# Performance work log

Hardware: AMD Instinct MI355X
Metric: run time of the kernel (lower is better)

Reference implementation:

```python
import jax, jax.numpy as jnp
import numpy as np

B, T, D, M = 4, 4096, 1024, 1024
EPS = 1e-6


def _rms_norm(x, w):
    return x * jax.lax.rsqrt(jnp.mean(x * x, axis=-1, keepdims=True) + EPS) * w


def _linrec(xg, r, h0):
    # h_t = x_t + r_t * h_{t-1}  (SRU-style linear recurrence, sqrll_kernel)
    def step(h, inp):
        xt, rt = inp
        h = xt + rt * h
        return h, h
    _, ys = jax.lax.scan(step, h0, (jnp.swapaxes(xg, 0, 1), jnp.swapaxes(r, 0, 1)))
    return jnp.swapaxes(ys, 0, 1)  # [B,T,M]


def setup_inputs() -> dict:
    key = jax.random.key(0)
    ks = jax.random.split(key, 16)
    s = 0.02
    return {
        "x": jax.random.normal(ks[0], (B, T, D), jnp.float32),
        "mem": jnp.zeros((B, M), jnp.float32),
        "norm_w": jnp.ones((D,), jnp.float32),
        "wr_w": jax.random.normal(ks[1], (M, D), jnp.float32) * s,
        "wr_b": jnp.zeros((M,), jnp.float32),
        "wi_w": jax.random.normal(ks[2], (M, D), jnp.float32) * s,
        "wig_w": jax.random.normal(ks[3], (M, D), jnp.float32) * s,
        "wig_b": jnp.zeros((M,), jnp.float32),
        "wog_w": jax.random.normal(ks[4], (M, D), jnp.float32) * s,
        "wog_b": jnp.zeros((M,), jnp.float32),
        "wo_w": jax.random.normal(ks[5], (D, M), jnp.float32) * s,
        "ffnorm_w": jnp.ones((D,), jnp.float32),
        "ffn_wi_w": jax.random.normal(ks[6], (M, D), jnp.float32) * s,
        "ffn_wg_w": jax.random.normal(ks[7], (M, D), jnp.float32) * s,
        "ffn_wg_b": jnp.zeros((M,), jnp.float32),
        "ffn_wo_w": jax.random.normal(ks[8], (D, M), jnp.float32) * s,
    }


def reference(x, mem, norm_w, wr_w, wr_b, wi_w, wig_w, wig_b, wog_w, wog_b,
              wo_w, ffnorm_w, ffn_wi_w, ffn_wg_w, ffn_wg_b, ffn_wo_w):
    # --- sqrll branch ---
    y = _rms_norm(x, norm_w)                                   # [B,T,D]
    ig = jax.nn.sigmoid(jnp.einsum('btd,md->btm', y, wig_w) + wig_b)
    og = jax.nn.sigmoid(jnp.einsum('btd,md->btm', y, wog_w) + wog_b)
    r = jax.nn.sigmoid(jnp.einsum('btd,md->btm', y, wr_w) + wr_b)
    xg = jnp.einsum('btd,md->btm', y, wi_w) * ig               # gated input
    h = _linrec(xg, r, mem)                                    # [B,T,M]
    mem_out = jax.lax.stop_gradient(h[:, -1])
    s = (h / (1.0 + jnp.abs(h))) * og                          # softsign * out gate
    x = x + jnp.einsum('btm,dm->btd', s, wo_w)                 # residual (dropout=0)
    # --- gated FFN branch ---
    z = _rms_norm(x, ffnorm_w)
    ff = jnp.einsum('btd,md->btm', z, ffn_wi_w) * jax.nn.sigmoid(
        jnp.einsum('btd,md->btm', z, ffn_wg_w) + ffn_wg_b)
    x = x + jnp.einsum('btm,dm->btd', ff, ffn_wo_w)
    return (x, mem_out)
```

## Files before the change

### kernel.cpp

```cpp
#include <hip/hip_runtime.h>
#include <stdint.h>


#define R_ROWS 16384
#define DIM    1024
#define MDIM   1024
#define TSEQ   4096
#define NCHUNK 128
#define TCH    32

typedef __attribute__((ext_vector_type(8))) short  bf16x8;
typedef __attribute__((ext_vector_type(8))) ushort u16x8;
typedef __attribute__((ext_vector_type(4))) float  f32x4;

__device__ __forceinline__ float bf2f(ushort u) {
  union { float f; unsigned int i; } x; x.i = ((unsigned int)u) << 16; return x.f;
}
__device__ __forceinline__ ushort f2bf(float f) {
  union { float f; unsigned int i; } x; x.f = f;
  unsigned int r = x.i + 0x7fffu + ((x.i >> 16) & 1u);
  return (ushort)(r >> 16);
}
__device__ __forceinline__ float sigmoidf_(float x) {
  return 1.0f / (1.0f + __expf(-x));
}
__device__ __forceinline__ void load_lds16(const void* g, void* s) {
  __builtin_amdgcn_global_load_lds(
      (const __attribute__((address_space(1))) void*)g,
      (__attribute__((address_space(3))) void*)s, 16, 0, 0);
}

#define AOFF(s,h) ((((s)*2)+(h))*8192)
#define BOFF(s,h) (49152 + (((s)*2)+(h))*8192)

__global__ __launch_bounds__(256)
void cvt_weights(const float* __restrict__ w0, const float* __restrict__ w1,
                 const float* __restrict__ w2, const float* __restrict__ w3,
                 const float* __restrict__ w4, const float* __restrict__ w5,
                 const float* __restrict__ w6, ushort* __restrict__ dst)
{
  const float* src; size_t base; int il;
  switch (blockIdx.y) {
    case 0: src = w0; base = 0;       il = 0; break;
    case 1: src = w1; base = 1048576; il = 0; break;
    case 2: src = w2; base = 2097152; il = 1; break;
    case 3: src = w3; base = 2097152; il = 2; break;
    case 4: src = w4; base = 5242880; il = 1; break;
    case 5: src = w5; base = 5242880; il = 2; break;
    default: src = w6; base = 4194304; il = 0; break;
  }
  const int i = blockIdx.x * 256 + threadIdx.x;
  const size_t e = (size_t)i * 4;
  size_t off;
  if (il == 0) off = base + e;
  else {
    const int row = (int)(e >> 10), col = (int)(e & 1023);
    const int nr = ((row >> 7) << 8) + (row & 127) + (il == 2 ? 128 : 0);
    off = base + (size_t)nr * 1024 + col;
  }
  const float4 v = *(const float4*)(src + e);
  ushort4 o; o.x = f2bf(v.x); o.y = f2bf(v.y); o.z = f2bf(v.z); o.w = f2bf(v.w);
  *(ushort4*)(dst + off) = o;
}

__global__ __launch_bounds__(256)
void cvt_one(const float* __restrict__ src, ushort* __restrict__ dst)
{
  const int i = blockIdx.x * 256 + threadIdx.x;
  const float4 v = *(const float4*)(src + (size_t)i * 4);
  ushort4 o; o.x = f2bf(v.x); o.y = f2bf(v.y); o.z = f2bf(v.z); o.w = f2bf(v.w);
  *(ushort4*)(dst + (size_t)i * 4) = o;
}

template<bool IN_F32>
__global__ __launch_bounds__(256)
void rmsnorm_k(const void* __restrict__ xin, const float* __restrict__ w,
               ushort* __restrict__ y)
{
  __shared__ float red[4];
  const int row = blockIdx.x;
  const int tid = threadIdx.x;
  const size_t base = (size_t)row * DIM + tid * 4;
  float v[4];
  if (IN_F32) {
    const float4 xv = *(const float4*)((const float*)xin + base);
    v[0] = xv.x; v[1] = xv.y; v[2] = xv.z; v[3] = xv.w;
  } else {
    const ushort4 xv = *(const ushort4*)((const ushort*)xin + base);
    v[0] = bf2f(xv.x); v[1] = bf2f(xv.y); v[2] = bf2f(xv.z); v[3] = bf2f(xv.w);
  }
  float ss = v[0]*v[0] + v[1]*v[1] + v[2]*v[2] + v[3]*v[3];
  for (int o = 32; o > 0; o >>= 1) ss += __shfl_down(ss, o, 64);
  const int wave = tid >> 6, lane = tid & 63;
  if (lane == 0) red[wave] = ss;
  __syncthreads();
  const float sum = red[0] + red[1] + red[2] + red[3];
  const float scale = rsqrtf(sum * (1.0f / DIM) + 1e-6f);
  const float4 wv = *(const float4*)(w + tid * 4);
  ushort4 o4;
  o4.x = f2bf(v[0] * scale * wv.x);
  o4.y = f2bf(v[1] * scale * wv.y);
  o4.z = f2bf(v[2] * scale * wv.z);
  o4.w = f2bf(v[3] * scale * wv.w);
  *(ushort4*)(y + base) = o4;
}

template<int MODE>
__global__ __launch_bounds__(512, 2)
void gemm8(const ushort* __restrict__ A, const ushort* __restrict__ W,
           const float* __restrict__ bias, const float* __restrict__ auxf,
           const ushort* __restrict__ auxb, ushort* __restrict__ outb,
           float* __restrict__ outf,
           const float* __restrict__ bias2, const float* __restrict__ bias3,
           ushort* __restrict__ outb2, ushort* __restrict__ outb3)
{
  __shared__ __align__(16) ushort lds[81920];
  const int tid  = threadIdx.x;
  const int bm = blockIdx.x, bn = blockIdx.y;
  const int wave = tid >> 6, lane = tid & 63;
  const int wm = wave >> 2, wn = wave & 3;
  const int quad = lane >> 4, l16 = lane & 15;
  const int axor = l16 & 7;

  const ushort* Ab = A + (size_t)bm * (256 * 1024);
  const ushort* Wb = W + (size_t)bn * (256 * 1024);

  f32x4 acc[8][4];
#pragma unroll
  for (int i = 0; i < 8; ++i)
#pragma unroll
    for (int j = 0; j < 4; ++j) acc[i][j] = (f32x4){0.f, 0.f, 0.f, 0.f};

  const int ci0 = tid, ci1 = tid + 512;
  const size_t gs0 = (size_t)(ci0 >> 3) * 1024 + (size_t)(((ci0 & 7) ^ ((ci0 >> 3) & 7)) << 3);
  const size_t gs1 = (size_t)(ci1 >> 3) * 1024 + (size_t)(((ci1 & 7) ^ ((ci1 >> 3) & 7)) << 3);
  auto stage = [&](const ushort* __restrict__ src, int loff) {
    load_lds16(src + gs0, &lds[loff + ci0 * 8]);
    load_lds16(src + gs1, &lds[loff + ci1 * 8]);
  };

  stage(Ab,               AOFF(0,0));
  stage(Ab + 131072,      AOFF(0,1));
  stage(Wb,               BOFF(0,0));
  stage(Wb + 131072,      BOFF(0,1));
  stage(Ab + 64,          AOFF(1,0));
  stage(Ab + 131072 + 64, AOFF(1,1));
  stage(Wb + 64,          BOFF(1,0));
  asm volatile("s_waitcnt vmcnt(6)" ::: "memory");
  __builtin_amdgcn_s_barrier();

  int kt3 = 0;
  for (int kt = 0; kt < 16; ++kt) {
    const ushort* Ah = &lds[AOFF(kt3, wm)];
    const ushort* Bh = &lds[BOFF(kt & 1, wn >> 1)];
    const int kt2s = (kt3 >= 1) ? kt3 - 1 : 2;
    const int brow0 = (wn & 1) * 64;
    bf16x8 bfr[4][2];
#pragma unroll
    for (int q = 0; q < 4; ++q) {
      if (q == 0) {
#pragma unroll
        for (int j = 0; j < 4; ++j)
#pragma unroll
          for (int ks = 0; ks < 2; ++ks)
            bfr[j][ks] = *(const bf16x8*)
                &Bh[(brow0 + j * 16 + l16) * 64 +
                    (((ks * 4 + quad) ^ axor) << 3)];
      }
      bf16x8 af[2][2];
#pragma unroll
      for (int p = 0; p < 2; ++p)
#pragma unroll
        for (int ks = 0; ks < 2; ++ks)
          af[p][ks] = *(const bf16x8*)
              &Ah[((2 * q + p) * 16 + l16) * 64 +
                  (((ks * 4 + quad) ^ axor) << 3)];
      if (q == 0 && kt + 1 < 16)
        stage(Wb + 131072 + (kt + 1) * 64, BOFF((kt + 1) & 1, 1));
      if (q == 1 && kt + 2 < 16)
        stage(Ab + (kt + 2) * 64,          AOFF(kt2s, 0));
      if (q == 2 && kt + 2 < 16)
        stage(Ab + 131072 + (kt + 2) * 64, AOFF(kt2s, 1));
      if (q == 3) {
        if (kt + 2 < 16)
          stage(Wb + (kt + 2) * 64,        BOFF(kt & 1, 0));
        if (kt < 14)       asm volatile("s_waitcnt vmcnt(6)" ::: "memory");
        else if (kt == 14) asm volatile("s_waitcnt vmcnt(0)" ::: "memory");
      }
      __builtin_amdgcn_s_barrier();
      asm volatile("s_waitcnt lgkmcnt(0)" ::: "memory");
      __builtin_amdgcn_s_setprio(1);
#pragma unroll
      for (int p = 0; p < 2; ++p)
#pragma unroll
        for (int j = 0; j < 4; ++j)
#pragma unroll
          for (int ks = 0; ks < 2; ++ks)
            acc[2 * q + p][j] = __builtin_amdgcn_mfma_f32_16x16x32_bf16(
                af[p][ks], bfr[j][ks], acc[2 * q + p][j], 0, 0, 0);
      __builtin_amdgcn_s_setprio(0);
    }
    kt3 = (kt3 == 2) ? 0 : kt3 + 1;
  }

  __builtin_amdgcn_s_barrier();
  float* C = (float*)lds;
  const bool gated = (MODE == 5) || (MODE == 6 && bn >= 8);
#pragma unroll 1
  for (int h = 0; h < 2; ++h) {
    if (wm == h) {
      const int cb = wn * 64;
#pragma unroll
      for (int i = 0; i < 8; ++i)
#pragma unroll
        for (int j = 0; j < 4; ++j)
#pragma unroll
          for (int g = 0; g < 4; ++g) {
            const int rw = i * 16 + quad * 4 + g;
            const int cw = cb + j * 16 + l16;
            C[rw * 256 + (cw ^ (((rw >> 2) & 1) << 4))] = acc[i][j][g];
          }
    }
    __syncthreads();
    if (gated) {
      const int outcol = (MODE == 6) ? (bn - 8) * 128 : bn * 128;
      const float* bp = (MODE == 6) ? bias3 : bias;
      ushort* ob = (MODE == 6) ? outb3 : outb;
#pragma unroll 1
      for (int sp = 0; sp < 4; ++sp) {
        const int lin = sp * 4096 + tid * 8;
        const int row = lin >> 7, c8 = lin & 127;
        const int xr = ((row >> 2) & 1) << 4;
        const int cg = c8 ^ xr;
        const int cv = (c8 + 128) ^ xr;
        const float4 gA = *(const float4*)&C[row * 256 + cg];
        const float4 gB = *(const float4*)&C[row * 256 + cg + 4];
        const float4 vA = *(const float4*)&C[row * 256 + cv];
        const float4 vB = *(const float4*)&C[row * 256 + cv + 4];
        const float4 b0 = *(const float4*)(bp + outcol + c8);
        const float4 b1 = *(const float4*)(bp + outcol + c8 + 4);
        const int rg = bm * 256 + h * 128 + row;
        const size_t gidx = (size_t)rg * 1024 + outcol + c8;
        u16x8 o;
        o[0] = f2bf(vA.x * sigmoidf_(gA.x + b0.x));
        o[1] = f2bf(vA.y * sigmoidf_(gA.y + b0.y));
        o[2] = f2bf(vA.z * sigmoidf_(gA.z + b0.z));
        o[3] = f2bf(vA.w * sigmoidf_(gA.w + b0.w));
        o[4] = f2bf(vB.x * sigmoidf_(gB.x + b1.x));
        o[5] = f2bf(vB.y * sigmoidf_(gB.y + b1.y));
        o[6] = f2bf(vB.z * sigmoidf_(gB.z + b1.z));
        o[7] = f2bf(vB.w * sigmoidf_(gB.w + b1.w));
        *(u16x8*)(ob + gidx) = o;
      }
    } else {
#pragma unroll 1
      for (int sp = 0; sp < 8; ++sp) {
        const int lin = sp * 4096 + tid * 8;
        const int row = lin >> 8, c8 = lin & 255;
        const int xr = ((row >> 2) & 1) << 4;
        const int cx = c8 ^ xr;
        const float4 vA = *(const float4*)&C[row * 256 + cx];
        const float4 vB = *(const float4*)&C[row * 256 + cx + 4];
        const int rg = bm * 256 + h * 128 + row;
        if (MODE == 6) {
          const int grp = bn >> 2;
          ushort* ob = grp ? outb2 : outb;
          const float* bp = grp ? bias2 : bias;
          const int colbase = (bn & 3) * 256;
          const size_t gidx = (size_t)rg * 1024 + colbase + c8;
          const float4 b0 = *(const float4*)(bp + colbase + c8);
          const float4 b1 = *(const float4*)(bp + colbase + c8 + 4);
          u16x8 o;
          o[0] = f2bf(sigmoidf_(vA.x + b0.x)); o[1] = f2bf(sigmoidf_(vA.y + b0.y));
          o[2] = f2bf(sigmoidf_(vA.z + b0.z)); o[3] = f2bf(sigmoidf_(vA.w + b0.w));
          o[4] = f2bf(sigmoidf_(vB.x + b1.x)); o[5] = f2bf(sigmoidf_(vB.y + b1.y));
          o[6] = f2bf(sigmoidf_(vB.z + b1.z)); o[7] = f2bf(sigmoidf_(vB.w + b1.w));
          *(u16x8*)(ob + gidx) = o;
        } else if (MODE == 1) {
          const size_t gidx = (size_t)rg * 1024 + bn * 256 + c8;
          const float4 a0 = *(const float4*)(auxf + gidx);
          const float4 a1 = *(const float4*)(auxf + gidx + 4);
          u16x8 o;
          o[0] = f2bf(vA.x + a0.x); o[1] = f2bf(vA.y + a0.y);
          o[2] = f2bf(vA.z + a0.z); o[3] = f2bf(vA.w + a0.w);
          o[4] = f2bf(vB.x + a1.x); o[5] = f2bf(vB.y + a1.y);
          o[6] = f2bf(vB.z + a1.z); o[7] = f2bf(vB.w + a1.w);
          *(u16x8*)(outb + gidx) = o;
        } else {
          const size_t gidx = (size_t)rg * 1024 + bn * 256 + c8;
          const u16x8 a8 = *(const u16x8*)(auxb + gidx);
          float4 o0, o1;
          o0.x = vA.x + bf2f(a8[0]); o0.y = vA.y + bf2f(a8[1]);
          o0.z = vA.z + bf2f(a8[2]); o0.w = vA.w + bf2f(a8[3]);
          o1.x = vB.x + bf2f(a8[4]); o1.y = vB.y + bf2f(a8[5]);
          o1.z = vB.z + bf2f(a8[6]); o1.w = vB.w + bf2f(a8[7]);
          *(float4*)(outf + gidx) = o0;
          *(float4*)(outf + gidx + 4) = o1;
        }
      }
    }
    if (h == 0) __syncthreads();
  }
}

__global__ __launch_bounds__(256)
void linrec_passA(ushort* __restrict__ xg, const ushort* __restrict__ r,
                  float* __restrict__ cL, float* __restrict__ cP)
{
  const int g = blockIdx.x * 256 + threadIdx.x;
  const int m4 = (g & 255) << 2;
  const int bc = g >> 8;
  const int b = bc >> 7, c = bc & 127;
  const size_t base = ((size_t)(b * TSEQ + c * TCH)) * MDIM + m4;
  float h0 = 0.f, h1 = 0.f, h2 = 0.f, h3 = 0.f;
  float p0 = 1.f, p1 = 1.f, p2 = 1.f, p3 = 1.f;
  for (int t = 0; t < TCH; ++t) {
    const size_t idx = base + (size_t)t * MDIM;
    const ushort4 xv = *(const ushort4*)&xg[idx];
    const ushort4 rv = *(const ushort4*)&r[idx];
    const float r0 = bf2f(rv.x), r1 = bf2f(rv.y), r2 = bf2f(rv.z), r3 = bf2f(rv.w);
    h0 = fmaf(r0, h0, bf2f(xv.x)); p0 *= r0;
    h1 = fmaf(r1, h1, bf2f(xv.y)); p1 *= r1;
    h2 = fmaf(r2, h2, bf2f(xv.z)); p2 *= r2;
    h3 = fmaf(r3, h3, bf2f(xv.w)); p3 *= r3;
    ushort4 o; o.x = f2bf(h0); o.y = f2bf(h1); o.z = f2bf(h2); o.w = f2bf(h3);
    *(ushort4*)&xg[idx] = o;
  }
  const size_t cb = (size_t)c * 4096 + b * MDIM + m4;
  float4 L4; L4.x = h0; L4.y = h1; L4.z = h2; L4.w = h3;
  float4 P4; P4.x = p0; P4.y = p1; P4.z = p2; P4.w = p3;
  *(float4*)&cL[cb] = L4;
  *(float4*)&cP[cb] = P4;
}

__global__ __launch_bounds__(256)
void linrec_passB(const float* __restrict__ cL, const float* __restrict__ cP,
                  const float* __restrict__ mem, float* __restrict__ cIn,
                  float* __restrict__ memout)
{
  const int g = blockIdx.x * 256 + threadIdx.x;
  float carry = mem[g];
#pragma unroll 4
  for (int c = 0; c < NCHUNK; ++c) {
    cIn[c * 4096 + g] = carry;
    carry = fmaf(cP[c * 4096 + g], carry, cL[c * 4096 + g]);
  }
  memout[g] = carry;
}

__global__ __launch_bounds__(256)
void linrec_passC(const ushort* __restrict__ L, const ushort* __restrict__ r,
                  const ushort* __restrict__ og, const float* __restrict__ cIn,
                  ushort* __restrict__ s)
{
  const int g = blockIdx.x * 256 + threadIdx.x;
  const int m4 = (g & 255) << 2;
  const int bc = g >> 8;
  const int b = bc >> 7, c = bc & 127;
  const size_t base = ((size_t)(b * TSEQ + c * TCH)) * MDIM + m4;
  const size_t cb = (size_t)c * 4096 + b * MDIM + m4;
  const float4 ci = *(const float4*)&cIn[cb];
  float p0 = 1.f, p1 = 1.f, p2 = 1.f, p3 = 1.f;
  for (int t = 0; t < TCH; ++t) {
    const size_t idx = base + (size_t)t * MDIM;
    const ushort4 rv = *(const ushort4*)&r[idx];
    const ushort4 lv = *(const ushort4*)&L[idx];
    const ushort4 ov = *(const ushort4*)&og[idx];
    p0 *= bf2f(rv.x); p1 *= bf2f(rv.y); p2 *= bf2f(rv.z); p3 *= bf2f(rv.w);
    const float a0 = fmaf(p0, ci.x, bf2f(lv.x));
    const float a1 = fmaf(p1, ci.y, bf2f(lv.y));
    const float a2 = fmaf(p2, ci.z, bf2f(lv.z));
    const float a3 = fmaf(p3, ci.w, bf2f(lv.w));
    ushort4 o;
    o.x = f2bf(a0 / (1.0f + fabsf(a0)) * bf2f(ov.x));
    o.y = f2bf(a1 / (1.0f + fabsf(a1)) * bf2f(ov.y));
    o.z = f2bf(a2 / (1.0f + fabsf(a2)) * bf2f(ov.z));
    o.w = f2bf(a3 / (1.0f + fabsf(a3)) * bf2f(ov.w));
    *(ushort4*)&s[idx] = o;
  }
}

extern "C" void kernel_launch(void* const* d_in, const int* in_sizes, int n_in,
                              void* d_out, int out_size, void* d_ws, size_t ws_size,
                              hipStream_t stream)
{
  const float* x        = (const float*)d_in[0];
  const float* mem      = (const float*)d_in[1];
  const float* norm_w   = (const float*)d_in[2];
  const float* wr_w     = (const float*)d_in[3];
  const float* wr_b     = (const float*)d_in[4];
  const float* wi_w     = (const float*)d_in[5];
  const float* wig_w    = (const float*)d_in[6];
  const float* wig_b    = (const float*)d_in[7];
  const float* wog_w    = (const float*)d_in[8];
  const float* wog_b    = (const float*)d_in[9];
  const float* wo_w     = (const float*)d_in[10];
  const float* ffnorm_w = (const float*)d_in[11];
  const float* ffn_wi_w = (const float*)d_in[12];
  const float* ffn_wg_w = (const float*)d_in[13];
  const float* ffn_wg_b = (const float*)d_in[14];
  const float* ffn_wo_w = (const float*)d_in[15];
  float* outF = (float*)d_out;

  ushort* xgL  = (ushort*)d_out;
  ushort* wbf  = (ushort*)((char*)d_out + 33554432ULL);
  float*  cL   = (float*)((char*)d_out + 48234496ULL);
  float*  cP   = (float*)((char*)d_out + 50331648ULL);
  float*  cIn  = (float*)((char*)d_out + 52428800ULL);
  float*  memoutF = outF + 16777216;

  char* ws = (char*)d_ws;
  ushort* y   = (ushort*)(ws);
  ushort* r   = (ushort*)(ws + 33554432ULL);
  ushort* og  = (ushort*)(ws + 67108864ULL);
  ushort* fwo_bf = (ushort*)(ws + 100663296ULL);
  ushort* s   = y;
  ushort* x1  = og;
  ushort* z   = r;
  ushort* gf  = y;

  cvt_weights<<<dim3(1024, 7), 256, 0, stream>>>(
      wr_w, wog_w, wig_w, wi_w, ffn_wg_w, ffn_wi_w, wo_w, wbf);
  cvt_one<<<1024, 256, 0, stream>>>(ffn_wo_w, fwo_bf);

  rmsnorm_k<true><<<R_ROWS, 256, 0, stream>>>(x, norm_w, y);
  gemm8<6><<<dim3(64, 16), 512, 0, stream>>>(
      y, wbf, wr_b, nullptr, nullptr, r, nullptr, wog_b, wig_b, og, xgL);
  linrec_passA<<<512, 256, 0, stream>>>(xgL, r, cL, cP);
  linrec_passB<<<16, 256, 0, stream>>>(cL, cP, mem, cIn, memoutF);
  linrec_passC<<<512, 256, 0, stream>>>(xgL, r, og, cIn, s);
  gemm8<1><<<dim3(64, 4), 512, 0, stream>>>(
      s, wbf + 4194304, nullptr, x, nullptr, x1, nullptr,
      nullptr, nullptr, nullptr, nullptr);
  rmsnorm_k<false><<<R_ROWS, 256, 0, stream>>>(x1, ffnorm_w, z);
  gemm8<5><<<dim3(64, 8), 512, 0, stream>>>(
      z, wbf + 5242880, ffn_wg_b, nullptr, nullptr, gf, nullptr,
      nullptr, nullptr, nullptr, nullptr);
  gemm8<3><<<dim3(64, 4), 512, 0, stream>>>(
      gf, fwo_bf, nullptr, nullptr, x1, nullptr, outF,
      nullptr, nullptr, nullptr, nullptr);
}
```

Measured before the change: 530.1 us.

## Switch GEMM to 32x32x16 MFMA, widen rmsnorm rows, merge weight conversion

The GEMM inner loop moves from 16x16x32 to 32x32x16 bf16 MFMA tiles. Fragment loads and the accumulator layout change to match, and the XOR swizzle in the epilogue LDS staging is dropped. The aim is fewer MFMA issues and LDS reads per FLOP, at the risk of LDS bank conflicts on the unswizzled C writes. Separately, rmsnorm processes two rows per block with 8-wide vectors, the two weight-conversion kernels are merged into one launch, and passB is relaunched with smaller blocks spread over more CUs.

```diff
diff --git a/kernel.cpp b/kernel.cpp
--- a/kernel.cpp
+++ b/kernel.cpp
@@ -9,9 +9,10 @@
 #define NCHUNK 128
 #define TCH    32
 
-typedef __attribute__((ext_vector_type(8))) short  bf16x8;
-typedef __attribute__((ext_vector_type(8))) ushort u16x8;
-typedef __attribute__((ext_vector_type(4))) float  f32x4;
+typedef __attribute__((ext_vector_type(8)))  short  bf16x8;
+typedef __attribute__((ext_vector_type(8)))  ushort u16x8;
+typedef __attribute__((ext_vector_type(4)))  float  f32x4;
+typedef __attribute__((ext_vector_type(16))) float  f32x16;
 
 __device__ __forceinline__ float bf2f(ushort u) {
   union { float f; unsigned int i; } x; x.i = ((unsigned int)u) << 16; return x.f;
@@ -37,9 +38,10 @@
 void cvt_weights(const float* __restrict__ w0, const float* __restrict__ w1,
                  const float* __restrict__ w2, const float* __restrict__ w3,
                  const float* __restrict__ w4, const float* __restrict__ w5,
-                 const float* __restrict__ w6, ushort* __restrict__ dst)
-{
-  const float* src; size_t base; int il;
+                 const float* __restrict__ w6, const float* __restrict__ w7,
+                 ushort* __restrict__ dst, ushort* __restrict__ dst2)
+{
+  const float* src; size_t base; int il; ushort* d = dst;
   switch (blockIdx.y) {
     case 0: src = w0; base = 0;       il = 0; break;
     case 1: src = w1; base = 1048576; il = 0; break;
@@ -47,7 +49,8 @@
     case 3: src = w3; base = 2097152; il = 2; break;
     case 4: src = w4; base = 5242880; il = 1; break;
     case 5: src = w5; base = 5242880; il = 2; break;
-    default: src = w6; base = 4194304; il = 0; break;
+    case 6: src = w6; base = 4194304; il = 0; break;
+    default: src = w7; base = 0; il = 0; d = dst2; break;
   }
   const int i = blockIdx.x * 256 + threadIdx.x;
   const size_t e = (size_t)i * 4;
@@ -60,16 +63,7 @@
   }
   const float4 v = *(const float4*)(src + e);
   ushort4 o; o.x = f2bf(v.x); o.y = f2bf(v.y); o.z = f2bf(v.z); o.w = f2bf(v.w);
-  *(ushort4*)(dst + off) = o;
-}
-
-__global__ __launch_bounds__(256)
-void cvt_one(const float* __restrict__ src, ushort* __restrict__ dst)
-{
-  const int i = blockIdx.x * 256 + threadIdx.x;
-  const float4 v = *(const float4*)(src + (size_t)i * 4);
-  ushort4 o; o.x = f2bf(v.x); o.y = f2bf(v.y); o.z = f2bf(v.z); o.w = f2bf(v.w);
-  *(ushort4*)(dst + (size_t)i * 4) = o;
+  *(ushort4*)(d + off) = o;
 }
 
 template<bool IN_F32>
@@ -78,31 +72,39 @@
                ushort* __restrict__ y)
 {
   __shared__ float red[4];
-  const int row = blockIdx.x;
   const int tid = threadIdx.x;
-  const size_t base = (size_t)row * DIM + tid * 4;
-  float v[4];
+  const int rh = tid >> 7;
+  const int rr = tid & 127;
+  const int row = blockIdx.x * 2 + rh;
+  const size_t base = (size_t)row * DIM + rr * 8;
+  float v[8];
   if (IN_F32) {
-    const float4 xv = *(const float4*)((const float*)xin + base);
-    v[0] = xv.x; v[1] = xv.y; v[2] = xv.z; v[3] = xv.w;
+    const float4 a = *(const float4*)((const float*)xin + base);
+    const float4 b = *(const float4*)((const float*)xin + base + 4);
+    v[0]=a.x; v[1]=a.y; v[2]=a.z; v[3]=a.w;
+    v[4]=b.x; v[5]=b.y; v[6]=b.z; v[7]=b.w;
   } else {
-    const ushort4 xv = *(const ushort4*)((const ushort*)xin + base);
-    v[0] = bf2f(xv.x); v[1] = bf2f(xv.y); v[2] = bf2f(xv.z); v[3] = bf2f(xv.w);
-  }
-  float ss = v[0]*v[0] + v[1]*v[1] + v[2]*v[2] + v[3]*v[3];
+    const u16x8 xv = *(const u16x8*)((const ushort*)xin + base);
+#pragma unroll
+    for (int i = 0; i < 8; ++i) v[i] = bf2f(xv[i]);
+  }
+  float ss = 0.f;
+#pragma unroll
+  for (int i = 0; i < 8; ++i) ss += v[i] * v[i];
   for (int o = 32; o > 0; o >>= 1) ss += __shfl_down(ss, o, 64);
-  const int wave = tid >> 6, lane = tid & 63;
-  if (lane == 0) red[wave] = ss;
+  const int wave = tid >> 6;
+  if ((tid & 63) == 0) red[wave] = ss;
   __syncthreads();
-  const float sum = red[0] + red[1] + red[2] + red[3];
+  const float sum = red[rh * 2] + red[rh * 2 + 1];
   const float scale = rsqrtf(sum * (1.0f / DIM) + 1e-6f);
-  const float4 wv = *(const float4*)(w + tid * 4);
-  ushort4 o4;
-  o4.x = f2bf(v[0] * scale * wv.x);
-  o4.y = f2bf(v[1] * scale * wv.y);
-  o4.z = f2bf(v[2] * scale * wv.z);
-  o4.w = f2bf(v[3] * scale * wv.w);
-  *(ushort4*)(y + base) = o4;
+  const float4 wa = *(const float4*)(w + rr * 8);
+  const float4 wb = *(const float4*)(w + rr * 8 + 4);
+  u16x8 o;
+  o[0] = f2bf(v[0] * scale * wa.x); o[1] = f2bf(v[1] * scale * wa.y);
+  o[2] = f2bf(v[2] * scale * wa.z); o[3] = f2bf(v[3] * scale * wa.w);
+  o[4] = f2bf(v[4] * scale * wb.x); o[5] = f2bf(v[5] * scale * wb.y);
+  o[6] = f2bf(v[6] * scale * wb.z); o[7] = f2bf(v[7] * scale * wb.w);
+  *(u16x8*)(y + base) = o;
 }
 
 template<int MODE>
@@ -119,17 +121,18 @@
   const int bm = blockIdx.x, bn = blockIdx.y;
   const int wave = tid >> 6, lane = tid & 63;
   const int wm = wave >> 2, wn = wave & 3;
-  const int quad = lane >> 4, l16 = lane & 15;
-  const int axor = l16 & 7;
+  const int l31 = lane & 31, lhi = lane >> 5, l7 = lane & 7;
 
   const ushort* Ab = A + (size_t)bm * (256 * 1024);
   const ushort* Wb = W + (size_t)bn * (256 * 1024);
 
-  f32x4 acc[8][4];
-#pragma unroll
-  for (int i = 0; i < 8; ++i)
-#pragma unroll
-    for (int j = 0; j < 4; ++j) acc[i][j] = (f32x4){0.f, 0.f, 0.f, 0.f};
+  f32x16 acc[4][2];
+#pragma unroll
+  for (int i = 0; i < 4; ++i)
+#pragma unroll
+    for (int j = 0; j < 2; ++j)
+#pragma unroll
+      for (int k = 0; k < 16; ++k) acc[i][j][k] = 0.f;
 
   const int ci0 = tid, ci1 = tid + 512;
   const size_t gs0 = (size_t)(ci0 >> 3) * 1024 + (size_t)(((ci0 & 7) ^ ((ci0 >> 3) & 7)) << 3);
@@ -155,26 +158,23 @@
     const ushort* Bh = &lds[BOFF(kt & 1, wn >> 1)];
     const int kt2s = (kt3 >= 1) ? kt3 - 1 : 2;
     const int brow0 = (wn & 1) * 64;
-    bf16x8 bfr[4][2];
+    bf16x8 bfa[4][2];
 #pragma unroll
     for (int q = 0; q < 4; ++q) {
       if (q == 0) {
 #pragma unroll
-        for (int j = 0; j < 4; ++j)
-#pragma unroll
-          for (int ks = 0; ks < 2; ++ks)
-            bfr[j][ks] = *(const bf16x8*)
-                &Bh[(brow0 + j * 16 + l16) * 64 +
-                    (((ks * 4 + quad) ^ axor) << 3)];
+        for (int qq = 0; qq < 4; ++qq)
+#pragma unroll
+          for (int nt = 0; nt < 2; ++nt)
+            bfa[qq][nt] = *(const bf16x8*)
+                &Bh[(brow0 + nt * 32 + l31) * 64 +
+                    (((qq * 2 + lhi) ^ l7) << 3)];
       }
-      bf16x8 af[2][2];
-#pragma unroll
-      for (int p = 0; p < 2; ++p)
-#pragma unroll
-        for (int ks = 0; ks < 2; ++ks)
-          af[p][ks] = *(const bf16x8*)
-              &Ah[((2 * q + p) * 16 + l16) * 64 +
-                  (((ks * 4 + quad) ^ axor) << 3)];
+      bf16x8 af[4];
+#pragma unroll
+      for (int mt = 0; mt < 4; ++mt)
+        af[mt] = *(const bf16x8*)
+            &Ah[(mt * 32 + l31) * 64 + (((q * 2 + lhi) ^ l7) << 3)];
       if (q == 0 && kt + 1 < 16)
         stage(Wb + 131072 + (kt + 1) * 64, BOFF((kt + 1) & 1, 1));
       if (q == 1 && kt + 2 < 16)
@@ -191,13 +191,11 @@
       asm volatile("s_waitcnt lgkmcnt(0)" ::: "memory");
       __builtin_amdgcn_s_setprio(1);
 #pragma unroll
-      for (int p = 0; p < 2; ++p)
-#pragma unroll
-        for (int j = 0; j < 4; ++j)
-#pragma unroll
-          for (int ks = 0; ks < 2; ++ks)
-            acc[2 * q + p][j] = __builtin_amdgcn_mfma_f32_16x16x32_bf16(
-                af[p][ks], bfr[j][ks], acc[2 * q + p][j], 0, 0, 0);
+      for (int mt = 0; mt < 4; ++mt)
+#pragma unroll
+        for (int nt = 0; nt < 2; ++nt)
+          acc[mt][nt] = __builtin_amdgcn_mfma_f32_32x32x16_bf16(
+              af[mt], bfa[q][nt], acc[mt][nt], 0, 0, 0);
       __builtin_amdgcn_s_setprio(0);
     }
     kt3 = (kt3 == 2) ? 0 : kt3 + 1;
@@ -211,15 +209,17 @@
     if (wm == h) {
       const int cb = wn * 64;
 #pragma unroll
-      for (int i = 0; i < 8; ++i)
-#pragma unroll
-        for (int j = 0; j < 4; ++j)
-#pragma unroll
-          for (int g = 0; g < 4; ++g) {
-            const int rw = i * 16 + quad * 4 + g;
-            const int cw = cb + j * 16 + l16;
-            C[rw * 256 + (cw ^ (((rw >> 2) & 1) << 4))] = acc[i][j][g];
-          }
+      for (int mt = 0; mt < 4; ++mt)
+#pragma unroll
+        for (int nt = 0; nt < 2; ++nt)
+#pragma unroll
+          for (int rq = 0; rq < 4; ++rq)
+#pragma unroll
+            for (int rr = 0; rr < 4; ++rr) {
+              const int rw = mt * 32 + rr + 8 * rq + 4 * lhi;
+              const int cw = cb + nt * 32 + l31;
+              C[rw * 256 + cw] = acc[mt][nt][rq * 4 + rr];
+            }
     }
     __syncthreads();
     if (gated) {
@@ -230,13 +230,10 @@
       for (int sp = 0; sp < 4; ++sp) {
         const int lin = sp * 4096 + tid * 8;
         const int row = lin >> 7, c8 = lin & 127;
-        const int xr = ((row >> 2) & 1) << 4;
-        const int cg = c8 ^ xr;
-        const int cv = (c8 + 128) ^ xr;
-        const float4 gA = *(const float4*)&C[row * 256 + cg];
-        const float4 gB = *(const float4*)&C[row * 256 + cg + 4];
-        const float4 vA = *(const float4*)&C[row * 256 + cv];
-        const float4 vB = *(const float4*)&C[row * 256 + cv + 4];
+        const float4 gA = *(const float4*)&C[row * 256 + c8];
+        const float4 gB = *(const float4*)&C[row * 256 + c8 + 4];
+        const float4 vA = *(const float4*)&C[row * 256 + c8 + 128];
+        const float4 vB = *(const float4*)&C[row * 256 + c8 + 132];
         const float4 b0 = *(const float4*)(bp + outcol + c8);
         const float4 b1 = *(const float4*)(bp + outcol + c8 + 4);
         const int rg = bm * 256 + h * 128 + row;
@@ -257,10 +254,8 @@
       for (int sp = 0; sp < 8; ++sp) {
         const int lin = sp * 4096 + tid * 8;
         const int row = lin >> 8, c8 = lin & 255;
-        const int xr = ((row >> 2) & 1) << 4;
-        const int cx = c8 ^ xr;
-        const float4 vA = *(const float4*)&C[row * 256 + cx];
-        const float4 vB = *(const float4*)&C[row * 256 + cx + 4];
+        const float4 vA = *(const float4*)&C[row * 256 + c8];
+        const float4 vB = *(const float4*)&C[row * 256 + c8 + 4];
         const int rg = bm * 256 + h * 128 + row;
         if (MODE == 6) {
           const int grp = bn >> 2;
@@ -333,12 +328,12 @@
   *(float4*)&cP[cb] = P4;
 }
 
-__global__ __launch_bounds__(256)
+__global__ __launch_bounds__(64)
 void linrec_passB(const float* __restrict__ cL, const float* __restrict__ cP,
                   const float* __restrict__ mem, float* __restrict__ cIn,
                   float* __restrict__ memout)
 {
-  const int g = blockIdx.x * 256 + threadIdx.x;
+  const int g = blockIdx.x * 64 + threadIdx.x;
   float carry = mem[g];
 #pragma unroll 4
   for (int c = 0; c < NCHUNK; ++c) {
@@ -419,20 +414,20 @@
   ushort* z   = r;
   ushort* gf  = y;
 
-  cvt_weights<<<dim3(1024, 7), 256, 0, stream>>>(
-      wr_w, wog_w, wig_w, wi_w, ffn_wg_w, ffn_wi_w, wo_w, wbf);
-  cvt_one<<<1024, 256, 0, stream>>>(ffn_wo_w, fwo_bf);
-
-  rmsnorm_k<true><<<R_ROWS, 256, 0, stream>>>(x, norm_w, y);
+  cvt_weights<<<dim3(1024, 8), 256, 0, stream>>>(
+      wr_w, wog_w, wig_w, wi_w, ffn_wg_w, ffn_wi_w, wo_w, ffn_wo_w,
+      wbf, fwo_bf);
+
+  rmsnorm_k<true><<<R_ROWS / 2, 256, 0, stream>>>(x, norm_w, y);
   gemm8<6><<<dim3(64, 16), 512, 0, stream>>>(
       y, wbf, wr_b, nullptr, nullptr, r, nullptr, wog_b, wig_b, og, xgL);
   linrec_passA<<<512, 256, 0, stream>>>(xgL, r, cL, cP);
-  linrec_passB<<<16, 256, 0, stream>>>(cL, cP, mem, cIn, memoutF);
+  linrec_passB<<<64, 64, 0, stream>>>(cL, cP, mem, cIn, memoutF);
   linrec_passC<<<512, 256, 0, stream>>>(xgL, r, og, cIn, s);
   gemm8<1><<<dim3(64, 4), 512, 0, stream>>>(
       s, wbf + 4194304, nullptr, x, nullptr, x1, nullptr,
       nullptr, nullptr, nullptr, nullptr);
-  rmsnorm_k<false><<<R_ROWS, 256, 0, stream>>>(x1, ffnorm_w, z);
+  rmsnorm_k<false><<<R_ROWS / 2, 256, 0, stream>>>(x1, ffnorm_w, z);
   gemm8<5><<<dim3(64, 8), 512, 0, stream>>>(
       z, wbf + 5242880, ffn_wg_b, nullptr, nullptr, gf, nullptr,
       nullptr, nullptr, nullptr, nullptr);
```

Result: slower. 548.7 us (+3.5%).
